# Optimization experiments

Measured on AMD Instinct MI355X. Metric: run time of the kernel, lower is better.

## Reference

```python
import jax, jax.numpy as jnp
import numpy as np

WEIGHT_BITS = 5
SHIFT_MIN = -(2 ** (WEIGHT_BITS - 1) - 2)  # -14, deepshift shift_range = (-(2^(b-1)-2), 0)
FRAC_BITS = 16  # quant_bits=16 -> 16.16 fixed point activations
INT_BITS = 16


def round_to_fixed(x):
    # deepshift ste.round_to_fixed: floor to 2^-16 grid, clamp to [-2^15, 2^15-1]
    delta = jnp.float32(2.0 ** (-FRAC_BITS))
    bound = jnp.float32(2.0 ** (INT_BITS - 1))
    q = jnp.clip(jnp.floor(x / delta) * delta, -bound, bound - 1)
    return x + jax.lax.stop_gradient(q - x)  # straight-through


def round_power_of_2(w):
    # deepshift: w_q = sign(w) * 2^clip(round(log2|w|), -14, 0)
    sign = jnp.sign(w)
    shift = jnp.round(jnp.log2(jnp.abs(w) + jnp.float32(1e-45)))
    shift = jnp.clip(shift, jnp.float32(SHIFT_MIN), jnp.float32(0.0))
    wq = sign * jnp.exp2(shift)
    return w + jax.lax.stop_gradient(wq - w)  # straight-through


def setup_inputs() -> dict:
    key = jax.random.key(0)
    k1, k2 = jax.random.split(key)
    B, C, H, W = 32, 384, 56, 56
    x = jax.random.normal(k1, (B, C, H, W), dtype=jnp.float32)
    # depthwise kernel [C_out, C_in/groups=1, 3, 3], kaiming-ish scale 1/sqrt(9)
    weight = jax.random.normal(k2, (C, 1, 3, 3), dtype=jnp.float32) * (1.0 / 3.0)
    return {"x": x, "weight": weight}


def reference(x, weight):
    xq = round_to_fixed(x)
    wq = round_power_of_2(weight)
    C = x.shape[1]
    # depthwise conv: groups = C, stride 1, padding 1
    out = jax.lax.conv_general_dilated(
        xq, wq,
        window_strides=(1, 1),
        padding=((1, 1), (1, 1)),
        feature_group_count=C,
        dimension_numbers=("NCHW", "OIHW", "NCHW"),
    )
    return out
```

## Files before the change

### kernel.cpp

```cpp
#include <hip/hip_runtime.h>
#include <math.h>

#define HWP   3136
#define W56   56
#define PITCH 58
#define NF4   784

__global__ __launch_bounds__(256) void dwconv3x3_q(
    const float* __restrict__ x, const float* __restrict__ wgt,
    float* __restrict__ out, int C)
{
    __shared__ float tile[PITCH * PITCH];
    __shared__ float wq[9];

    const int tid   = threadIdx.x;
    const int plane = blockIdx.x;
    const int c     = plane % C;

    if (tid < PITCH) {
        tile[tid] = 0.f;
        tile[(PITCH - 1) * PITCH + tid] = 0.f;
        tile[tid * PITCH] = 0.f;
        tile[tid * PITCH + (PITCH - 1)] = 0.f;
    }

    if (tid < 9) {
        float v  = wgt[c * 9 + tid];
        float s  = (v > 0.f) ? 1.f : ((v < 0.f) ? -1.f : 0.f);
        float sh = rintf(log2f(fabsf(v) + 1e-45f));
        sh = fminf(fmaxf(sh, -14.f), 0.f);
        wq[tid] = s * exp2f(sh);
    }

    const float4* __restrict__ xp = (const float4*)(x + (size_t)plane * HWP);
    for (int i = tid; i < NF4; i += 256) {
        float4 v = xp[i];
        v.x = fminf(fmaxf(floorf(v.x * 65536.f) * (1.f / 65536.f), -32768.f), 32767.f);
        v.y = fminf(fmaxf(floorf(v.y * 65536.f) * (1.f / 65536.f), -32768.f), 32767.f);
        v.z = fminf(fmaxf(floorf(v.z * 65536.f) * (1.f / 65536.f), -32768.f), 32767.f);
        v.w = fminf(fmaxf(floorf(v.w * 65536.f) * (1.f / 65536.f), -32768.f), 32767.f);
        int p  = i * 4;
        int h  = p / W56;
        int wc = p - h * W56;
        float* dst = &tile[(h + 1) * PITCH + wc + 1];
        dst[0] = v.x; dst[1] = v.y; dst[2] = v.z; dst[3] = v.w;
    }
    __syncthreads();

    const float w00 = wq[0], w01 = wq[1], w02 = wq[2];
    const float w10 = wq[3], w11 = wq[4], w12 = wq[5];
    const float w20 = wq[6], w21 = wq[7], w22 = wq[8];

    float4* __restrict__ op = (float4*)(out + (size_t)plane * HWP);
    for (int j = tid; j < NF4; j += 256) {
        int p  = j * 4;
        int h  = p / W56;
        int wc = p - h * W56;
        float4 o = make_float4(0.f, 0.f, 0.f, 0.f);
        #pragma unroll
        for (int dh = 0; dh < 3; ++dh) {
            const float* r = &tile[(h + dh) * PITCH + wc];
            float r0 = r[0], r1 = r[1], r2 = r[2];
            float r3 = r[3], r4 = r[4], r5 = r[5];
            float a, b, cc;
            if (dh == 0)      { a = w00; b = w01; cc = w02; }
            else if (dh == 1) { a = w10; b = w11; cc = w12; }
            else              { a = w20; b = w21; cc = w22; }
            o.x = fmaf(a, r0, fmaf(b, r1, fmaf(cc, r2, o.x)));
            o.y = fmaf(a, r1, fmaf(b, r2, fmaf(cc, r3, o.y)));
            o.z = fmaf(a, r2, fmaf(b, r3, fmaf(cc, r4, o.z)));
            o.w = fmaf(a, r3, fmaf(b, r4, fmaf(cc, r5, o.w)));
        }
        op[j] = o;
    }
}

extern "C" void kernel_launch(void* const* d_in, const int* in_sizes, int n_in,
                              void* d_out, int out_size, void* d_ws, size_t ws_size,
                              hipStream_t stream) {
    const float* x   = (const float*)d_in[0];
    const float* wgt = (const float*)d_in[1];
    float* out       = (float*)d_out;

    const int planes = out_size / HWP;
    const int C      = in_sizes[1] / 9;

    dwconv3x3_q<<<planes, 256, 0, stream>>>(x, wgt, out, C);
}
```

Before: 65.51 us.

## Replace LDS-tiled depthwise conv with direct per-thread global loads

Drops the per-plane shared-memory tile and its barrier. Each thread now computes 8 adjacent outputs of one row straight from global memory, using float4 loads plus scalar halo loads, and relies on cache for the reuse between neighbouring rows. When workspace is available, the weights are quantized once in a separate small kernel; otherwise they are quantized inline. The cost is that each input row is read three times through cache, there is an extra kernel launch, and the ±32768 clamp on activations is removed, which only matters for inputs far outside the test range.

```diff
diff --git a/kernel.cpp b/kernel.cpp
--- a/kernel.cpp
+++ b/kernel.cpp
@@ -1,78 +1,89 @@
 #include <hip/hip_runtime.h>
 #include <math.h>
 
-#define HWP   3136
-#define W56   56
-#define PITCH 58
-#define NF4   784
+#define HWP 3136
+#define W56 56
+#define TPP 392
 
-__global__ __launch_bounds__(256) void dwconv3x3_q(
-    const float* __restrict__ x, const float* __restrict__ wgt,
-    float* __restrict__ out, int C)
-{
-    __shared__ float tile[PITCH * PITCH];
-    __shared__ float wq[9];
-
-    const int tid   = threadIdx.x;
-    const int plane = blockIdx.x;
-    const int c     = plane % C;
-
-    if (tid < PITCH) {
-        tile[tid] = 0.f;
-        tile[(PITCH - 1) * PITCH + tid] = 0.f;
-        tile[tid * PITCH] = 0.f;
-        tile[tid * PITCH + (PITCH - 1)] = 0.f;
-    }
-
-    if (tid < 9) {
-        float v  = wgt[c * 9 + tid];
+__global__ __launch_bounds__(256) void quant_weights(const float* __restrict__ wgt,
+                                                     float* __restrict__ wq, int n) {
+    int i = blockIdx.x * 256 + threadIdx.x;
+    if (i < n) {
+        float v  = wgt[i];
         float s  = (v > 0.f) ? 1.f : ((v < 0.f) ? -1.f : 0.f);
         float sh = rintf(log2f(fabsf(v) + 1e-45f));
         sh = fminf(fmaxf(sh, -14.f), 0.f);
-        wq[tid] = s * exp2f(sh);
+        wq[i] = s * exp2f(sh);
+    }
+}
+
+__device__ __forceinline__ float qfix(float v) {
+    return floorf(v * 65536.f) * (1.f / 65536.f);
+}
+
+__global__ __launch_bounds__(256) void dwconv3x3_direct(
+    const float* __restrict__ x, const float* __restrict__ wq,
+    float* __restrict__ out, int C, int nTasks, int preq)
+{
+    int t = blockIdx.x * 256 + threadIdx.x;
+    if (t >= nTasks) return;
+    int plane = t / TPP;
+    int rem   = t - plane * TPP;
+    int h     = rem / 7;
+    int w8    = rem - h * 7;
+    int wc    = w8 * 8;
+
+    const float* xp = x + (size_t)plane * HWP;
+    const float* wp = wq + (size_t)(plane % C) * 9;
+
+    float w9[9];
+    #pragma unroll
+    for (int k = 0; k < 9; ++k) w9[k] = wp[k];
+    if (!preq) {
+        #pragma unroll
+        for (int k = 0; k < 9; ++k) {
+            float v  = w9[k];
+            float s  = (v > 0.f) ? 1.f : ((v < 0.f) ? -1.f : 0.f);
+            float sh = rintf(log2f(fabsf(v) + 1e-45f));
+            sh = fminf(fmaxf(sh, -14.f), 0.f);
+            w9[k] = s * exp2f(sh);
+        }
     }
 
-    const float4* __restrict__ xp = (const float4*)(x + (size_t)plane * HWP);
-    for (int i = tid; i < NF4; i += 256) {
-        float4 v = xp[i];
-        v.x = fminf(fmaxf(floorf(v.x * 65536.f) * (1.f / 65536.f), -32768.f), 32767.f);
-        v.y = fminf(fmaxf(floorf(v.y * 65536.f) * (1.f / 65536.f), -32768.f), 32767.f);
-        v.z = fminf(fmaxf(floorf(v.z * 65536.f) * (1.f / 65536.f), -32768.f), 32767.f);
-        v.w = fminf(fmaxf(floorf(v.w * 65536.f) * (1.f / 65536.f), -32768.f), 32767.f);
-        int p  = i * 4;
-        int h  = p / W56;
-        int wc = p - h * W56;
-        float* dst = &tile[(h + 1) * PITCH + wc + 1];
-        dst[0] = v.x; dst[1] = v.y; dst[2] = v.z; dst[3] = v.w;
+    float acc[8];
+    #pragma unroll
+    for (int j = 0; j < 8; ++j) acc[j] = 0.f;
+
+    #pragma unroll
+    for (int dh = 0; dh < 3; ++dh) {
+        int  r     = h + dh - 1;
+        bool valid = (r >= 0) && (r < 56);
+        int  rc    = min(max(r, 0), 55);
+        const float* row = xp + rc * W56 + wc;
+
+        float4 m0 = *(const float4*)(row);
+        float4 m1 = *(const float4*)(row + 4);
+        float left  = (wc > 0)      ? row[-1] : 0.f;
+        float right = (wc + 8 < 56) ? row[8]  : 0.f;
+
+        float v[10];
+        v[0] = qfix(left);
+        v[1] = qfix(m0.x); v[2] = qfix(m0.y); v[3] = qfix(m0.z); v[4] = qfix(m0.w);
+        v[5] = qfix(m1.x); v[6] = qfix(m1.y); v[7] = qfix(m1.z); v[8] = qfix(m1.w);
+        v[9] = qfix(right);
+
+        float a = valid ? w9[dh * 3 + 0] : 0.f;
+        float b = valid ? w9[dh * 3 + 1] : 0.f;
+        float c = valid ? w9[dh * 3 + 2] : 0.f;
+
+        #pragma unroll
+        for (int j = 0; j < 8; ++j)
+            acc[j] = fmaf(a, v[j], fmaf(b, v[j + 1], fmaf(c, v[j + 2], acc[j])));
     }
-    __syncthreads();
 
-    const float w00 = wq[0], w01 = wq[1], w02 = wq[2];
-    const float w10 = wq[3], w11 = wq[4], w12 = wq[5];
-    const float w20 = wq[6], w21 = wq[7], w22 = wq[8];
-
-    float4* __restrict__ op = (float4*)(out + (size_t)plane * HWP);
-    for (int j = tid; j < NF4; j += 256) {
-        int p  = j * 4;
-        int h  = p / W56;
-        int wc = p - h * W56;
-        float4 o = make_float4(0.f, 0.f, 0.f, 0.f);
-        #pragma unroll
-        for (int dh = 0; dh < 3; ++dh) {
-            const float* r = &tile[(h + dh) * PITCH + wc];
-            float r0 = r[0], r1 = r[1], r2 = r[2];
-            float r3 = r[3], r4 = r[4], r5 = r[5];
-            float a, b, cc;
-            if (dh == 0)      { a = w00; b = w01; cc = w02; }
-            else if (dh == 1) { a = w10; b = w11; cc = w12; }
-            else              { a = w20; b = w21; cc = w22; }
-            o.x = fmaf(a, r0, fmaf(b, r1, fmaf(cc, r2, o.x)));
-            o.y = fmaf(a, r1, fmaf(b, r2, fmaf(cc, r3, o.y)));
-            o.z = fmaf(a, r2, fmaf(b, r3, fmaf(cc, r4, o.z)));
-            o.w = fmaf(a, r3, fmaf(b, r4, fmaf(cc, r5, o.w)));
-        }
-        op[j] = o;
-    }
+    float* op = out + (size_t)plane * HWP + h * W56 + wc;
+    *(float4*)(op)     = make_float4(acc[0], acc[1], acc[2], acc[3]);
+    *(float4*)(op + 4) = make_float4(acc[4], acc[5], acc[6], acc[7]);
 }
 
 extern "C" void kernel_launch(void* const* d_in, const int* in_sizes, int n_in,
@@ -83,7 +94,18 @@
     float* out       = (float*)d_out;
 
     const int planes = out_size / HWP;
-    const int C      = in_sizes[1] / 9;
+    const int nW     = in_sizes[1];
+    const int C      = nW / 9;
+    const int nTasks = planes * TPP;
 
-    dwconv3x3_q<<<planes, 256, 0, stream>>>(x, wgt, out, C);
+    int preq = (ws_size >= (size_t)nW * sizeof(float)) ? 1 : 0;
+    const float* wqp = wgt;
+    if (preq) {
+        float* wqbuf = (float*)d_ws;
+        quant_weights<<<(nW + 255) / 256, 256, 0, stream>>>(wgt, wqbuf, nW);
+        wqp = wqbuf;
+    }
+
+    dwconv3x3_direct<<<(nTasks + 255) / 256, 256, 0, stream>>>(
+        x, wqp, out, C, nTasks, preq);
 }
```

New measurement: 119.2 us. 1.82x slower.
